# Kernel tuning notes

Measured on AMD Instinct MI355X. Metric: run time of the kernel, lower is better.

## Reference

```python
import jax, jax.numpy as jnp
import numpy as np

N = 100000      # nodes
E = 600000      # directed edges
D_IN = 128
D_H = 128
D_OUT = 128
EPS = 1e-5      # BatchNorm eps


def setup_inputs() -> dict:
    key = jax.random.key(0)
    ks = jax.random.split(key, 6)
    x = jax.random.normal(ks[0], (N, D_IN), dtype=jnp.float32)
    edge_index = jax.random.randint(ks[1], (2, E), 0, N, dtype=jnp.int64)
    s1 = 1.0 / np.sqrt(D_IN)
    s2 = 1.0 / np.sqrt(D_H)
    W1 = jax.random.uniform(ks[2], (D_IN, D_H), minval=-s1, maxval=s1, dtype=jnp.float32)
    b1 = jnp.zeros((D_H,), jnp.float32)
    gamma1 = jnp.ones((D_H,), jnp.float32)
    beta1 = jnp.zeros((D_H,), jnp.float32)
    W2 = jax.random.uniform(ks[3], (D_H, D_OUT), minval=-s2, maxval=s2, dtype=jnp.float32)
    b2 = jnp.zeros((D_OUT,), jnp.float32)
    return dict(x=x, edge_index=edge_index, W1=W1, b1=b1,
                gamma1=gamma1, beta1=beta1, W2=W2, b2=b2)


def _gcn_conv(x, W, b, src, dst):
    # PyG GCNConv: h = D^{-1/2} (A + I) D^{-1/2} (x @ W) + b
    n = x.shape[0]
    h = x @ W                                   # [N, d_out]
    loop = jnp.arange(n, dtype=src.dtype)
    s = jnp.concatenate([src, loop])            # self loops appended
    d = jnp.concatenate([dst, loop])
    deg = jax.ops.segment_sum(jnp.ones_like(d, jnp.float32), d, num_segments=n)
    dinv = jax.lax.rsqrt(deg)                   # deg >= 1 after self loops
    norm = dinv[s] * dinv[d]                    # [E + N]
    agg = jax.ops.segment_sum(h[s] * norm[:, None], d, num_segments=n)  # [N, d_out]
    return agg + b


def reference(x, edge_index, W1, b1, gamma1, beta1, W2, b2):
    src, dst = edge_index[0], edge_index[1]
    # layer 0: GCNConv -> BatchNorm1d (training batch stats) -> ReLU (dropout p=0)
    h = _gcn_conv(x, W1, b1, src, dst)
    mean = h.mean(axis=0)
    var = h.var(axis=0)                         # biased variance, as torch BN
    h = (h - mean) * jax.lax.rsqrt(var + EPS) * gamma1 + beta1
    h = jax.nn.relu(h)
    # final layer: GCNConv only
    return _gcn_conv(h, W2, b2, src, dst)
```

## Files before the change

### kernel.cpp

```cpp
#include <hip/hip_runtime.h>

#define D 128
#define EPSV 1e-5f

typedef __attribute__((ext_vector_type(8))) short bf16x8;
typedef __attribute__((ext_vector_type(4))) float f32x4;

__device__ __forceinline__ short f2bf(float f){
  unsigned u = __float_as_uint(f);
  u += 0x7fffu + ((u >> 16) & 1u);
  return (short)(u >> 16);
}
__device__ __forceinline__ float bflo(unsigned u){ return __uint_as_float(u << 16); }
__device__ __forceinline__ float bfhi(unsigned u){ return __uint_as_float(u & 0xffff0000u); }
__device__ __forceinline__ float bf2f(short s){ return __uint_as_float(((unsigned)(unsigned short)s) << 16); }
__device__ __forceinline__ unsigned packbf(float a, float b){
  unsigned lo = (unsigned short)f2bf(a);
  unsigned hi = (unsigned short)f2bf(b);
  return lo | (hi << 16);
}

__global__ void k_init(int N, int E, const int* __restrict__ ei, int* __restrict__ flag,
                       int* __restrict__ deg, int* __restrict__ fill, float* __restrict__ gpart,
                       const float* __restrict__ W1, const float* __restrict__ W2,
                       short* __restrict__ w1t, short* __restrict__ w2t){
  int i = blockIdx.x*blockDim.x + threadIdx.x;
  if (i < N){ deg[i] = 0; fill[i] = 0; }
  if (i < D*D){
    int j = i >> 7, k = i & 127;
    w1t[i] = f2bf(W1[k*D + j]);
    w2t[i] = f2bf(W2[k*D + j]);
  }
  if (i < 2048) gpart[i] = 0.f;
  if (blockIdx.x == 0){
    __shared__ int any;
    int t = threadIdx.x;
    if (t == 0) any = 0;
    __syncthreads();
    if (2*t+1 < 2*E && ei[2*t+1] != 0) atomicOr(&any, 1);
    __syncthreads();
    if (t == 0) flag[0] = (any == 0) ? 1 : 0;
  }
}

__global__ void k_count(const int* __restrict__ ei, int E, const int* __restrict__ flag,
                        int* __restrict__ deg){
  int e = blockIdx.x*blockDim.x + threadIdx.x;
  if (e >= E) return;
  int d = flag[0] ? ei[2*E + 2*e] : ei[E + e];
  atomicAdd(&deg[d], 1);
}

__global__ void k_dinv_bsum(const int* __restrict__ deg, int N, float* __restrict__ dinv,
                            int* __restrict__ bsum){
  __shared__ int sh[256];
  int t = threadIdx.x, base = blockIdx.x*1024;
  int s = 0;
  for (int i = t; i < 1024; i += 256){
    int j = base + i;
    if (j < N){ int dg = deg[j]; dinv[j] = rsqrtf((float)(dg + 1)); s += dg; }
  }
  sh[t] = s; __syncthreads();
  for (int d = 128; d > 0; d >>= 1){ if (t < d) sh[t] += sh[t+d]; __syncthreads(); }
  if (t == 0) bsum[blockIdx.x] = sh[0];
}

__global__ void k_scan_bsum(int NB, const int* __restrict__ bsum, int* __restrict__ boff){
  __shared__ int sh[128];
  int t = threadIdx.x;
  int v = (t < NB) ? bsum[t] : 0;
  sh[t] = v; __syncthreads();
  for (int d = 1; d < 128; d <<= 1){
    int u = (t >= d) ? sh[t-d] : 0;
    __syncthreads();
    sh[t] += u;
    __syncthreads();
  }
  if (t < NB) boff[t] = sh[t] - v;
}

__global__ void k_rowptr(const int* __restrict__ deg, int N, const int* __restrict__ boff,
                         int* __restrict__ row_ptr){
  __shared__ int sh[256];
  int t = threadIdx.x;
  int base = blockIdx.x*1024 + t*4;
  int c0 = (base+0 < N) ? deg[base+0] : 0;
  int c1 = (base+1 < N) ? deg[base+1] : 0;
  int c2 = (base+2 < N) ? deg[base+2] : 0;
  int c3 = (base+3 < N) ? deg[base+3] : 0;
  int s = c0 + c1 + c2 + c3;
  sh[t] = s; __syncthreads();
  for (int d = 1; d < 256; d <<= 1){
    int v = (t >= d) ? sh[t-d] : 0;
    __syncthreads();
    sh[t] += v;
    __syncthreads();
  }
  int o = sh[t] - s + boff[blockIdx.x];
  if (base+0 < N) row_ptr[base+0] = o; o += c0;
  if (base+1 < N) row_ptr[base+1] = o; o += c1;
  if (base+2 < N) row_ptr[base+2] = o; o += c2;
  if (base+3 < N) row_ptr[base+3] = o;
}

__global__ void k_scatter(const int* __restrict__ ei, int E, const int* __restrict__ flag,
                          const int* __restrict__ rowp, int* __restrict__ fill,
                          const float* __restrict__ dinv, int2* __restrict__ epack){
  int e = blockIdx.x*blockDim.x + threadIdx.x;
  if (e >= E) return;
  int s, d;
  if (flag[0]){ s = ei[2*e]; d = ei[2*E + 2*e]; }
  else        { s = ei[e];   d = ei[E + e];     }
  int pos = rowp[d] + atomicAdd(&fill[d], 1);
  int2 ev; ev.x = s; ev.y = __float_as_int(dinv[s] * dinv[d]);
  epack[pos] = ev;
}

template<int MODE>
__global__ __launch_bounds__(256, 2) void k_gemm(const void* __restrict__ A,
                                const short* __restrict__ BT, short* __restrict__ C, int N,
                                const float* __restrict__ scale, const float* __restrict__ shift){
  __shared__ short ldsB[16384];
  __shared__ short ldsC[4*2048];
  int w = threadIdx.x >> 6;
  int lane = threadIdx.x & 63;
  int m = lane & 15, quad = lane >> 4;

  {
    const bf16x8* BTv = (const bf16x8*)BT;
    bf16x8* Bw = (bf16x8*)ldsB;
    for (int g = threadIdx.x; g < 2048; g += 256){
      int row = g >> 4, ch = g & 15;
      Bw[row*16 + (ch ^ (row & 15))] = BTv[g];
    }
  }
  __syncthreads();
  const bf16x8* Bv = (const bf16x8*)ldsB;
  short* cw = ldsC + w*2048;

  int tiles = (N + 31) >> 5;
  int wid = blockIdx.x*4 + w;
  int wstride = gridDim.x*4;
  for (int tile = wid; tile < tiles; tile += wstride){
    int r0 = tile << 5;
    bf16x8 a[2][4];
    #pragma unroll
    for (int g = 0; g < 2; ++g){
      int row = r0 + g*16 + m;
      if (row >= N) row = N - 1;
      #pragma unroll
      for (int kc = 0; kc < 4; ++kc){
        int k0 = kc*32 + quad*8;
        if (MODE == 1){
          const float* Af = (const float*)A + (size_t)row*D + k0;
          float4 u = *(const float4*)Af;
          float4 v = *(const float4*)(Af + 4);
          bf16x8 tv;
          tv[0]=f2bf(u.x); tv[1]=f2bf(u.y); tv[2]=f2bf(u.z); tv[3]=f2bf(u.w);
          tv[4]=f2bf(v.x); tv[5]=f2bf(v.y); tv[6]=f2bf(v.z); tv[7]=f2bf(v.w);
          a[g][kc] = tv;
        } else {
          bf16x8 raw = *(const bf16x8*)((const short*)A + (size_t)row*D + k0);
          float4 s0v = *(const float4*)(scale + k0);
          float4 s1v = *(const float4*)(scale + k0 + 4);
          float4 h0v = *(const float4*)(shift + k0);
          float4 h1v = *(const float4*)(shift + k0 + 4);
          bf16x8 tv;
          tv[0] = f2bf(fmaxf(fmaf(bf2f(raw[0]), s0v.x, h0v.x), 0.f));
          tv[1] = f2bf(fmaxf(fmaf(bf2f(raw[1]), s0v.y, h0v.y), 0.f));
          tv[2] = f2bf(fmaxf(fmaf(bf2f(raw[2]), s0v.z, h0v.z), 0.f));
          tv[3] = f2bf(fmaxf(fmaf(bf2f(raw[3]), s0v.w, h0v.w), 0.f));
          tv[4] = f2bf(fmaxf(fmaf(bf2f(raw[4]), s1v.x, h1v.x), 0.f));
          tv[5] = f2bf(fmaxf(fmaf(bf2f(raw[5]), s1v.y, h1v.y), 0.f));
          tv[6] = f2bf(fmaxf(fmaf(bf2f(raw[6]), s1v.z, h1v.z), 0.f));
          tv[7] = f2bf(fmaxf(fmaf(bf2f(raw[7]), s1v.w, h1v.w), 0.f));
          a[g][kc] = tv;
        }
      }
    }
    f32x4 acc[2][8];
    #pragma unroll
    for (int g = 0; g < 2; ++g)
      #pragma unroll
      for (int c = 0; c < 8; ++c) acc[g][c] = (f32x4){0.f,0.f,0.f,0.f};
    #pragma unroll
    for (int kc = 0; kc < 4; ++kc){
      bf16x8 bb[8];
      #pragma unroll
      for (int c = 0; c < 8; ++c)
        bb[c] = Bv[(c*16 + m)*16 + ((kc*4 + quad) ^ m)];
      #pragma unroll
      for (int g = 0; g < 2; ++g)
        #pragma unroll
        for (int c = 0; c < 8; ++c)
          acc[g][c] = __builtin_amdgcn_mfma_f32_16x16x32_bf16(bb[c], a[g][kc], acc[g][c], 0, 0, 0);
    }
    #pragma unroll
    for (int g = 0; g < 2; ++g){
      #pragma unroll
      for (int c = 0; c < 8; ++c){
        uint2 v;
        v.x = packbf(acc[g][c][0], acc[g][c][1]);
        v.y = packbf(acc[g][c][2], acc[g][c][3]);
        int x = c*2 + (quad >> 1);
        *(uint2*)&cw[m*128 + ((x ^ m) << 3) + ((quad & 1) << 2)] = v;
      }
      asm volatile("s_waitcnt lgkmcnt(0)" ::: "memory");
      #pragma unroll
      for (int rg = 0; rg < 4; ++rg){
        int lrow = rg*4 + quad;
        int rr = r0 + g*16 + lrow;
        uint4 v = *(const uint4*)&cw[lrow*128 + ((m ^ lrow) << 3)];
        if (rr < N) *(uint4*)(C + (size_t)rr*D + m*8) = v;
      }
      asm volatile("s_waitcnt lgkmcnt(0)" ::: "memory");
    }
  }
}

template<int OUTF32>
__global__ __launch_bounds__(256) void k_agg(const short* __restrict__ H, const int* __restrict__ rowp,
        const int* __restrict__ deg, const int2* __restrict__ epack, const float* __restrict__ dinv,
        const float* __restrict__ bias, void* __restrict__ out, int N, float* __restrict__ gpart){
  int w = threadIdx.x >> 6, p = threadIdx.x & 63;
  int wid = blockIdx.x*4 + w, wstride = gridDim.x*4;
  const unsigned* Hu = (const unsigned*)H;
  float S0=0.f, S1=0.f, Q0=0.f, Q1=0.f;
  for (int n = wid; n < N; n += wstride){
    float d1 = dinv[n], w0 = d1*d1;
    unsigned u = Hu[(size_t)n*64 + p];
    float a0 = w0 * bflo(u), a1 = w0 * bfhi(u);
    int start = rowp[n], cnt = deg[n];
    for (int base = 0; base < cnt; base += 64){
      int nb = cnt - base; if (nb > 64) nb = 64;
      int2 ev;
      if (p < nb) ev = epack[start + base + p];
      else { ev.x = 0; ev.y = 0; }
      for (int j = 0; j < nb; j += 8){
        int s0 = __shfl(ev.x, j+0), s1 = __shfl(ev.x, j+1);
        int s2 = __shfl(ev.x, j+2), s3 = __shfl(ev.x, j+3);
        int s4 = __shfl(ev.x, j+4), s5 = __shfl(ev.x, j+5);
        int s6 = __shfl(ev.x, j+6), s7 = __shfl(ev.x, j+7);
        float f0 = __int_as_float(__shfl(ev.y, j+0));
        float f1 = __int_as_float(__shfl(ev.y, j+1));
        float f2 = __int_as_float(__shfl(ev.y, j+2));
        float f3 = __int_as_float(__shfl(ev.y, j+3));
        float f4 = __int_as_float(__shfl(ev.y, j+4));
        float f5 = __int_as_float(__shfl(ev.y, j+5));
        float f6 = __int_as_float(__shfl(ev.y, j+6));
        float f7 = __int_as_float(__shfl(ev.y, j+7));
        unsigned u0 = Hu[(size_t)s0*64 + p], u1 = Hu[(size_t)s1*64 + p];
        unsigned u2 = Hu[(size_t)s2*64 + p], u3 = Hu[(size_t)s3*64 + p];
        unsigned u4 = Hu[(size_t)s4*64 + p], u5 = Hu[(size_t)s5*64 + p];
        unsigned u6 = Hu[(size_t)s6*64 + p], u7 = Hu[(size_t)s7*64 + p];
        a0 = fmaf(f0, bflo(u0), a0); a1 = fmaf(f0, bfhi(u0), a1);
        a0 = fmaf(f1, bflo(u1), a0); a1 = fmaf(f1, bfhi(u1), a1);
        a0 = fmaf(f2, bflo(u2), a0); a1 = fmaf(f2, bfhi(u2), a1);
        a0 = fmaf(f3, bflo(u3), a0); a1 = fmaf(f3, bfhi(u3), a1);
        a0 = fmaf(f4, bflo(u4), a0); a1 = fmaf(f4, bfhi(u4), a1);
        a0 = fmaf(f5, bflo(u5), a0); a1 = fmaf(f5, bfhi(u5), a1);
        a0 = fmaf(f6, bflo(u6), a0); a1 = fmaf(f6, bfhi(u6), a1);
        a0 = fmaf(f7, bflo(u7), a0); a1 = fmaf(f7, bfhi(u7), a1);
      }
    }
    if (OUTF32){
      float2 r; r.x = a0 + bias[2*p]; r.y = a1 + bias[2*p+1];
      ((float2*)out)[(size_t)n*64 + p] = r;
    } else {
      ((unsigned*)out)[(size_t)n*64 + p] = packbf(a0, a1);
      S0 += a0; Q0 += a0*a0; S1 += a1; Q1 += a1*a1;
    }
  }
  if (!OUTF32){
    __shared__ float ls[1024];
    int base = w*256;
    ls[base + 2*p]       = S0;
    ls[base + 2*p + 1]   = S1;
    ls[base + 128 + 2*p]     = Q0;
    ls[base + 128 + 2*p + 1] = Q1;
    __syncthreads();
    int t = threadIdx.x;
    float v = ls[t] + ls[256 + t] + ls[512 + t] + ls[768 + t];
    atomicAdd(&gpart[(blockIdx.x & 7)*256 + t], v);
  }
}

__global__ void k_ss(const float* __restrict__ gpart, const float* __restrict__ gamma,
                     const float* __restrict__ beta, int N,
                     float* __restrict__ scale, float* __restrict__ shift){
  int f = threadIdx.x;
  if (f < 128){
    float s = 0.f, q = 0.f;
    for (int i = 0; i < 8; ++i){ s += gpart[i*256 + f]; q += gpart[i*256 + 128 + f]; }
    float inv = 1.f / (float)N;
    float mean = s * inv;
    float var  = q * inv - mean*mean;
    float sc = gamma[f] * rsqrtf(var + EPSV);
    scale[f] = sc;
    shift[f] = beta[f] - mean * sc;
  }
}

extern "C" void kernel_launch(void* const* d_in, const int* in_sizes, int n_in,
                              void* d_out, int out_size, void* d_ws, size_t ws_size,
                              hipStream_t stream){
  const float* x   = (const float*)d_in[0];
  const int*   ei  = (const int*)  d_in[1];
  const float* W1  = (const float*)d_in[2];
  const float* g1  = (const float*)d_in[4];
  const float* be1 = (const float*)d_in[5];
  const float* W2  = (const float*)d_in[6];
  const float* b2  = (const float*)d_in[7];
  float* out = (float*)d_out;
  int N = in_sizes[0] / D;
  int E = in_sizes[1] / 2;

  char* w = (char*)d_ws;
  auto carve = [&](size_t bytes)->char*{ char* p = w; w += (bytes + 255) & ~(size_t)255; return p; };
  int*   flag  = (int*)  carve(256);
  int*   degA  = (int*)  carve((size_t)N*4);
  int*   fillA = (int*)  carve((size_t)N*4);
  float* dinvA = (float*)carve((size_t)N*4);
  int*   rowp  = (int*)  carve((size_t)N*4);
  int*   bsum  = (int*)  carve(4096);
  int*   boff  = (int*)  carve(4096);
  int2*  epack = (int2*) carve((size_t)E*8);
  float* gpart = (float*)carve(2048*4);
  float* scale = (float*)carve(512);
  float* shift = (float*)carve(512);
  short* w1t   = (short*)carve((size_t)D*D*2);
  short* w2t   = (short*)carve((size_t)D*D*2);
  short* h1    = (short*)carve((size_t)N*D*2);
  short* hb    = (short*)carve((size_t)N*D*2);

  const int TB = 256;
  int EB  = (E + TB - 1) / TB;
  int NBt = (N + TB - 1) / TB;
  int NB1024 = (N + 1023) / 1024;
  int GEMMB = 512;
  int AGGB  = 2048;

  k_init      <<<NBt, TB, 0, stream>>>(N, E, ei, flag, degA, fillA, gpart, W1, W2, w1t, w2t);
  k_count     <<<EB, TB, 0, stream>>>(ei, E, flag, degA);
  k_dinv_bsum <<<NB1024, 256, 0, stream>>>(degA, N, dinvA, bsum);
  k_scan_bsum <<<1, 128, 0, stream>>>(NB1024, bsum, boff);
  k_rowptr    <<<NB1024, 256, 0, stream>>>(degA, N, boff, rowp);
  k_scatter   <<<EB, TB, 0, stream>>>(ei, E, flag, rowp, fillA, dinvA, epack);
  k_gemm<1>   <<<GEMMB, 256, 0, stream>>>(x, w1t, h1, N, nullptr, nullptr);
  k_agg<0>    <<<AGGB, 256, 0, stream>>>(h1, rowp, degA, epack, dinvA, nullptr, hb, N, gpart);
  k_ss        <<<1, 128, 0, stream>>>(gpart, g1, be1, N, scale, shift);
  k_gemm<2>   <<<GEMMB, 256, 0, stream>>>(hb, w2t, h1, N, scale, shift);
  k_agg<1>    <<<AGGB, 256, 0, stream>>>(h1, rowp, degA, epack, dinvA, b2, out, N, gpart);
}
```

Baseline: 266.1 us.

## Fuse degree count into GEMM, single-pass lookback scan, inline BN stats, prefetch agg rows

Extra blocks in the first GEMM launch now do the degree counting, so the atomics overlap the dense GEMM. The three-kernel row-pointer scan becomes one decoupled-lookback scan that also writes dinv. The BN scale and shift are computed per block inside the second GEMM, which removes k_ss. The aggregation loop now prefetches the next node's row metadata and first edge chunk. The changes cut launch count and expose more latency overlap, at the cost of spin-waiting across blocks in the scan and redundant BN stat work in every GEMM block.

```diff
diff --git a/kernel.cpp b/kernel.cpp
--- a/kernel.cpp
+++ b/kernel.cpp
@@ -22,6 +22,7 @@
 
 __global__ void k_init(int N, int E, const int* __restrict__ ei, int* __restrict__ flag,
                        int* __restrict__ deg, int* __restrict__ fill, float* __restrict__ gpart,
+                       int* __restrict__ sflg,
                        const float* __restrict__ W1, const float* __restrict__ W2,
                        short* __restrict__ w1t, short* __restrict__ w2t){
   int i = blockIdx.x*blockDim.x + threadIdx.x;
@@ -32,6 +33,7 @@
     w2t[i] = f2bf(W2[k*D + j]);
   }
   if (i < 2048) gpart[i] = 0.f;
+  if (i < 128) sflg[i] = 0;
   if (blockIdx.x == 0){
     __shared__ int any;
     int t = threadIdx.x;
@@ -43,47 +45,13 @@
   }
 }
 
-__global__ void k_count(const int* __restrict__ ei, int E, const int* __restrict__ flag,
-                        int* __restrict__ deg){
-  int e = blockIdx.x*blockDim.x + threadIdx.x;
-  if (e >= E) return;
-  int d = flag[0] ? ei[2*E + 2*e] : ei[E + e];
-  atomicAdd(&deg[d], 1);
-}
-
-__global__ void k_dinv_bsum(const int* __restrict__ deg, int N, float* __restrict__ dinv,
-                            int* __restrict__ bsum){
+__global__ void k_scan(const int* __restrict__ deg, int N, int* __restrict__ rowp,
+                       float* __restrict__ dinv, int* __restrict__ s_agg,
+                       int* __restrict__ s_inc, int* __restrict__ s_flg){
   __shared__ int sh[256];
-  int t = threadIdx.x, base = blockIdx.x*1024;
-  int s = 0;
-  for (int i = t; i < 1024; i += 256){
-    int j = base + i;
-    if (j < N){ int dg = deg[j]; dinv[j] = rsqrtf((float)(dg + 1)); s += dg; }
-  }
-  sh[t] = s; __syncthreads();
-  for (int d = 128; d > 0; d >>= 1){ if (t < d) sh[t] += sh[t+d]; __syncthreads(); }
-  if (t == 0) bsum[blockIdx.x] = sh[0];
-}
-
-__global__ void k_scan_bsum(int NB, const int* __restrict__ bsum, int* __restrict__ boff){
-  __shared__ int sh[128];
-  int t = threadIdx.x;
-  int v = (t < NB) ? bsum[t] : 0;
-  sh[t] = v; __syncthreads();
-  for (int d = 1; d < 128; d <<= 1){
-    int u = (t >= d) ? sh[t-d] : 0;
-    __syncthreads();
-    sh[t] += u;
-    __syncthreads();
-  }
-  if (t < NB) boff[t] = sh[t] - v;
-}
-
-__global__ void k_rowptr(const int* __restrict__ deg, int N, const int* __restrict__ boff,
-                         int* __restrict__ row_ptr){
-  __shared__ int sh[256];
-  int t = threadIdx.x;
-  int base = blockIdx.x*1024 + t*4;
+  __shared__ int s_ex;
+  int b = blockIdx.x, t = threadIdx.x;
+  int base = b*1024 + t*4;
   int c0 = (base+0 < N) ? deg[base+0] : 0;
   int c1 = (base+1 < N) ? deg[base+1] : 0;
   int c2 = (base+2 < N) ? deg[base+2] : 0;
@@ -96,11 +64,29 @@
     sh[t] += v;
     __syncthreads();
   }
-  int o = sh[t] - s + boff[blockIdx.x];
-  if (base+0 < N) row_ptr[base+0] = o; o += c0;
-  if (base+1 < N) row_ptr[base+1] = o; o += c1;
-  if (base+2 < N) row_ptr[base+2] = o; o += c2;
-  if (base+3 < N) row_ptr[base+3] = o;
+  int total = sh[255];
+  if (t == 0){
+    atomicExch(&s_agg[b], total);
+    __threadfence();
+    atomicExch(&s_flg[b], 1);
+    int ex = 0;
+    for (int i = b-1; i >= 0; ){
+      int f;
+      while ((f = atomicAdd(&s_flg[i], 0)) == 0) __builtin_amdgcn_s_sleep(1);
+      if (f == 2){ ex += atomicAdd(&s_inc[i], 0); break; }
+      ex += atomicAdd(&s_agg[i], 0); --i;
+    }
+    atomicExch(&s_inc[b], ex + total);
+    __threadfence();
+    atomicExch(&s_flg[b], 2);
+    s_ex = ex;
+  }
+  __syncthreads();
+  int o = sh[t] - s + s_ex;
+  if (base+0 < N){ rowp[base+0] = o; dinv[base+0] = rsqrtf((float)(c0+1)); } o += c0;
+  if (base+1 < N){ rowp[base+1] = o; dinv[base+1] = rsqrtf((float)(c1+1)); } o += c1;
+  if (base+2 < N){ rowp[base+2] = o; dinv[base+2] = rsqrtf((float)(c2+1)); } o += c2;
+  if (base+3 < N){ rowp[base+3] = o; dinv[base+3] = rsqrtf((float)(c3+1)); }
 }
 
 __global__ void k_scatter(const int* __restrict__ ei, int E, const int* __restrict__ flag,
@@ -119,13 +105,44 @@
 template<int MODE>
 __global__ __launch_bounds__(256, 2) void k_gemm(const void* __restrict__ A,
                                 const short* __restrict__ BT, short* __restrict__ C, int N,
-                                const float* __restrict__ scale, const float* __restrict__ shift){
+                                const float* __restrict__ gpart, const float* __restrict__ gamma,
+                                const float* __restrict__ beta,
+                                const int* __restrict__ ei, int E, const int* __restrict__ flag,
+                                int* __restrict__ deg, int ngemmb){
+  if (MODE == 1 && (int)blockIdx.x >= ngemmb){
+    int cb = blockIdx.x - ngemmb;
+    int e0 = cb*1024 + threadIdx.x;
+    int f = flag[0];
+    #pragma unroll
+    for (int r = 0; r < 4; ++r){
+      int e = e0 + r*256;
+      if (e < E){
+        int d = f ? ei[2*E + 2*e] : ei[E + e];
+        atomicAdd(&deg[d], 1);
+      }
+    }
+    return;
+  }
   __shared__ short ldsB[16384];
   __shared__ short ldsC[4*2048];
+  __shared__ __align__(16) float s_sc[128];
+  __shared__ __align__(16) float s_sh[128];
   int w = threadIdx.x >> 6;
   int lane = threadIdx.x & 63;
   int m = lane & 15, quad = lane >> 4;
 
+  if (MODE == 2 && threadIdx.x < 128){
+    int f = threadIdx.x;
+    float s = 0.f, q = 0.f;
+    #pragma unroll
+    for (int i = 0; i < 8; ++i){ s += gpart[i*256 + f]; q += gpart[i*256 + 128 + f]; }
+    float inv = 1.f / (float)N;
+    float mean = s * inv;
+    float var  = q * inv - mean*mean;
+    float sc = gamma[f] * rsqrtf(var + EPSV);
+    s_sc[f] = sc;
+    s_sh[f] = beta[f] - mean * sc;
+  }
   {
     const bf16x8* BTv = (const bf16x8*)BT;
     bf16x8* Bw = (bf16x8*)ldsB;
@@ -140,7 +157,7 @@
 
   int tiles = (N + 31) >> 5;
   int wid = blockIdx.x*4 + w;
-  int wstride = gridDim.x*4;
+  int wstride = ngemmb*4;
   for (int tile = wid; tile < tiles; tile += wstride){
     int r0 = tile << 5;
     bf16x8 a[2][4];
@@ -161,10 +178,10 @@
           a[g][kc] = tv;
         } else {
           bf16x8 raw = *(const bf16x8*)((const short*)A + (size_t)row*D + k0);
-          float4 s0v = *(const float4*)(scale + k0);
-          float4 s1v = *(const float4*)(scale + k0 + 4);
-          float4 h0v = *(const float4*)(shift + k0);
-          float4 h1v = *(const float4*)(shift + k0 + 4);
+          float4 s0v = *(const float4*)(s_sc + k0);
+          float4 s1v = *(const float4*)(s_sc + k0 + 4);
+          float4 h0v = *(const float4*)(s_sh + k0);
+          float4 h1v = *(const float4*)(s_sh + k0 + 4);
           bf16x8 tv;
           tv[0] = f2bf(fmaxf(fmaf(bf2f(raw[0]), s0v.x, h0v.x), 0.f));
           tv[1] = f2bf(fmaxf(fmaf(bf2f(raw[1]), s0v.y, h0v.y), 0.f));
@@ -226,50 +243,77 @@
   int wid = blockIdx.x*4 + w, wstride = gridDim.x*4;
   const unsigned* Hu = (const unsigned*)H;
   float S0=0.f, S1=0.f, Q0=0.f, Q1=0.f;
-  for (int n = wid; n < N; n += wstride){
-    float d1 = dinv[n], w0 = d1*d1;
-    unsigned u = Hu[(size_t)n*64 + p];
+  float bb0=0.f, bb1=0.f;
+  if (OUTF32){ bb0 = bias[2*p]; bb1 = bias[2*p+1]; }
+
+  int n = wid;
+  int start=0, cnt=0; float d1=0.f; unsigned u=0; int2 ev; ev.x=0; ev.y=0;
+  if (n < N){
+    start = rowp[n]; cnt = deg[n]; d1 = dinv[n];
+    u = Hu[(size_t)n*64 + p];
+    int nb = cnt < 64 ? cnt : 64;
+    if (p < nb) ev = epack[start + p];
+  }
+  while (n < N){
+    int n2 = n + wstride;
+    int start2=0, cnt2=0; float d12=0.f; unsigned u2=0; int2 ev2; ev2.x=0; ev2.y=0;
+    if (n2 < N){
+      start2 = rowp[n2]; cnt2 = deg[n2]; d12 = dinv[n2];
+      u2 = Hu[(size_t)n2*64 + p];
+      int nb2 = cnt2 < 64 ? cnt2 : 64;
+      if (p < nb2) ev2 = epack[start2 + p];
+    }
+    float w0 = d1*d1;
     float a0 = w0 * bflo(u), a1 = w0 * bfhi(u);
-    int start = rowp[n], cnt = deg[n];
-    for (int base = 0; base < cnt; base += 64){
-      int nb = cnt - base; if (nb > 64) nb = 64;
-      int2 ev;
-      if (p < nb) ev = epack[start + base + p];
-      else { ev.x = 0; ev.y = 0; }
-      for (int j = 0; j < nb; j += 8){
-        int s0 = __shfl(ev.x, j+0), s1 = __shfl(ev.x, j+1);
-        int s2 = __shfl(ev.x, j+2), s3 = __shfl(ev.x, j+3);
-        int s4 = __shfl(ev.x, j+4), s5 = __shfl(ev.x, j+5);
-        int s6 = __shfl(ev.x, j+6), s7 = __shfl(ev.x, j+7);
-        float f0 = __int_as_float(__shfl(ev.y, j+0));
-        float f1 = __int_as_float(__shfl(ev.y, j+1));
-        float f2 = __int_as_float(__shfl(ev.y, j+2));
-        float f3 = __int_as_float(__shfl(ev.y, j+3));
-        float f4 = __int_as_float(__shfl(ev.y, j+4));
-        float f5 = __int_as_float(__shfl(ev.y, j+5));
-        float f6 = __int_as_float(__shfl(ev.y, j+6));
-        float f7 = __int_as_float(__shfl(ev.y, j+7));
-        unsigned u0 = Hu[(size_t)s0*64 + p], u1 = Hu[(size_t)s1*64 + p];
-        unsigned u2 = Hu[(size_t)s2*64 + p], u3 = Hu[(size_t)s3*64 + p];
-        unsigned u4 = Hu[(size_t)s4*64 + p], u5 = Hu[(size_t)s5*64 + p];
-        unsigned u6 = Hu[(size_t)s6*64 + p], u7 = Hu[(size_t)s7*64 + p];
-        a0 = fmaf(f0, bflo(u0), a0); a1 = fmaf(f0, bfhi(u0), a1);
-        a0 = fmaf(f1, bflo(u1), a0); a1 = fmaf(f1, bfhi(u1), a1);
-        a0 = fmaf(f2, bflo(u2), a0); a1 = fmaf(f2, bfhi(u2), a1);
-        a0 = fmaf(f3, bflo(u3), a0); a1 = fmaf(f3, bfhi(u3), a1);
-        a0 = fmaf(f4, bflo(u4), a0); a1 = fmaf(f4, bfhi(u4), a1);
-        a0 = fmaf(f5, bflo(u5), a0); a1 = fmaf(f5, bfhi(u5), a1);
-        a0 = fmaf(f6, bflo(u6), a0); a1 = fmaf(f6, bfhi(u6), a1);
-        a0 = fmaf(f7, bflo(u7), a0); a1 = fmaf(f7, bfhi(u7), a1);
+    int nb = cnt < 64 ? cnt : 64;
+    for (int j = 0; j < nb; j += 8){
+      int s0 = __shfl(ev.x, j+0), s1 = __shfl(ev.x, j+1);
+      int s2 = __shfl(ev.x, j+2), s3 = __shfl(ev.x, j+3);
+      int s4 = __shfl(ev.x, j+4), s5 = __shfl(ev.x, j+5);
+      int s6 = __shfl(ev.x, j+6), s7 = __shfl(ev.x, j+7);
+      float f0 = __int_as_float(__shfl(ev.y, j+0));
+      float f1 = __int_as_float(__shfl(ev.y, j+1));
+      float f2 = __int_as_float(__shfl(ev.y, j+2));
+      float f3 = __int_as_float(__shfl(ev.y, j+3));
+      float f4 = __int_as_float(__shfl(ev.y, j+4));
+      float f5 = __int_as_float(__shfl(ev.y, j+5));
+      float f6 = __int_as_float(__shfl(ev.y, j+6));
+      float f7 = __int_as_float(__shfl(ev.y, j+7));
+      unsigned u0 = Hu[(size_t)s0*64 + p], u1 = Hu[(size_t)s1*64 + p];
+      unsigned u2g = Hu[(size_t)s2*64 + p], u3 = Hu[(size_t)s3*64 + p];
+      unsigned u4 = Hu[(size_t)s4*64 + p], u5 = Hu[(size_t)s5*64 + p];
+      unsigned u6 = Hu[(size_t)s6*64 + p], u7 = Hu[(size_t)s7*64 + p];
+      a0 = fmaf(f0, bflo(u0), a0); a1 = fmaf(f0, bfhi(u0), a1);
+      a0 = fmaf(f1, bflo(u1), a0); a1 = fmaf(f1, bfhi(u1), a1);
+      a0 = fmaf(f2, bflo(u2g), a0); a1 = fmaf(f2, bfhi(u2g), a1);
+      a0 = fmaf(f3, bflo(u3), a0); a1 = fmaf(f3, bfhi(u3), a1);
+      a0 = fmaf(f4, bflo(u4), a0); a1 = fmaf(f4, bfhi(u4), a1);
+      a0 = fmaf(f5, bflo(u5), a0); a1 = fmaf(f5, bfhi(u5), a1);
+      a0 = fmaf(f6, bflo(u6), a0); a1 = fmaf(f6, bfhi(u6), a1);
+      a0 = fmaf(f7, bflo(u7), a0); a1 = fmaf(f7, bfhi(u7), a1);
+    }
+    for (int base = 64; base < cnt; base += 64){
+      int nbx = cnt - base; if (nbx > 64) nbx = 64;
+      int2 evx; evx.x = 0; evx.y = 0;
+      if (p < nbx) evx = epack[start + base + p];
+      for (int j = 0; j < nbx; j += 8){
+        #pragma unroll
+        for (int q2 = 0; q2 < 8; ++q2){
+          int sx = __shfl(evx.x, j+q2);
+          float fx = __int_as_float(__shfl(evx.y, j+q2));
+          unsigned ux = Hu[(size_t)sx*64 + p];
+          a0 = fmaf(fx, bflo(ux), a0); a1 = fmaf(fx, bfhi(ux), a1);
+        }
       }
     }
     if (OUTF32){
-      float2 r; r.x = a0 + bias[2*p]; r.y = a1 + bias[2*p+1];
+      float2 r; r.x = a0 + bb0; r.y = a1 + bb1;
       ((float2*)out)[(size_t)n*64 + p] = r;
     } else {
       ((unsigned*)out)[(size_t)n*64 + p] = packbf(a0, a1);
       S0 += a0; Q0 += a0*a0; S1 += a1; Q1 += a1*a1;
     }
+    n = n2; start = start2; cnt = cnt2; d1 = d12; u = u2; ev = ev2;
   }
   if (!OUTF32){
     __shared__ float ls[1024];
@@ -282,22 +326,6 @@
     int t = threadIdx.x;
     float v = ls[t] + ls[256 + t] + ls[512 + t] + ls[768 + t];
     atomicAdd(&gpart[(blockIdx.x & 7)*256 + t], v);
-  }
-}
-
-__global__ void k_ss(const float* __restrict__ gpart, const float* __restrict__ gamma,
-                     const float* __restrict__ beta, int N,
-                     float* __restrict__ scale, float* __restrict__ shift){
-  int f = threadIdx.x;
-  if (f < 128){
-    float s = 0.f, q = 0.f;
-    for (int i = 0; i < 8; ++i){ s += gpart[i*256 + f]; q += gpart[i*256 + 128 + f]; }
-    float inv = 1.f / (float)N;
-    float mean = s * inv;
-    float var  = q * inv - mean*mean;
-    float sc = gamma[f] * rsqrtf(var + EPSV);
-    scale[f] = sc;
-    shift[f] = beta[f] - mean * sc;
   }
 }
 
@@ -322,12 +350,11 @@
   int*   fillA = (int*)  carve((size_t)N*4);
   float* dinvA = (float*)carve((size_t)N*4);
   int*   rowp  = (int*)  carve((size_t)N*4);
-  int*   bsum  = (int*)  carve(4096);
-  int*   boff  = (int*)  carve(4096);
+  int*   sagg  = (int*)  carve(512);
+  int*   sinc  = (int*)  carve(512);
+  int*   sflg  = (int*)  carve(512);
   int2*  epack = (int2*) carve((size_t)E*8);
   float* gpart = (float*)carve(2048*4);
-  float* scale = (float*)carve(512);
-  float* shift = (float*)carve(512);
   short* w1t   = (short*)carve((size_t)D*D*2);
   short* w2t   = (short*)carve((size_t)D*D*2);
   short* h1    = (short*)carve((size_t)N*D*2);
@@ -338,17 +365,16 @@
   int NBt = (N + TB - 1) / TB;
   int NB1024 = (N + 1023) / 1024;
   int GEMMB = 512;
+  int CNTB  = (E + 1023) / 1024;
   int AGGB  = 2048;
 
-  k_init      <<<NBt, TB, 0, stream>>>(N, E, ei, flag, degA, fillA, gpart, W1, W2, w1t, w2t);
-  k_count     <<<EB, TB, 0, stream>>>(ei, E, flag, degA);
-  k_dinv_bsum <<<NB1024, 256, 0, stream>>>(degA, N, dinvA, bsum);
-  k_scan_bsum <<<1, 128, 0, stream>>>(NB1024, bsum, boff);
-  k_rowptr    <<<NB1024, 256, 0, stream>>>(degA, N, boff, rowp);
-  k_scatter   <<<EB, TB, 0, stream>>>(ei, E, flag, rowp, fillA, dinvA, epack);
-  k_gemm<1>   <<<GEMMB, 256, 0, stream>>>(x, w1t, h1, N, nullptr, nullptr);
-  k_agg<0>    <<<AGGB, 256, 0, stream>>>(h1, rowp, degA, epack, dinvA, nullptr, hb, N, gpart);
-  k_ss        <<<1, 128, 0, stream>>>(gpart, g1, be1, N, scale, shift);
-  k_gemm<2>   <<<GEMMB, 256, 0, stream>>>(hb, w2t, h1, N, scale, shift);
-  k_agg<1>    <<<AGGB, 256, 0, stream>>>(h1, rowp, degA, epack, dinvA, b2, out, N, gpart);
-}
+  k_init    <<<NBt, TB, 0, stream>>>(N, E, ei, flag, degA, fillA, gpart, sflg, W1, W2, w1t, w2t);
+  k_gemm<1> <<<GEMMB + CNTB, 256, 0, stream>>>(x, w1t, h1, N, nullptr, nullptr, nullptr,
+                                               ei, E, flag, degA, GEMMB);
+  k_scan    <<<NB1024, 256, 0, stream>>>(degA, N, rowp, dinvA, sagg, sinc, sflg);
+  k_scatter <<<EB, TB, 0, stream>>>(ei, E, flag, rowp, fillA, dinvA, epack);
+  k_agg<0>  <<<AGGB, 256, 0, stream>>>(h1, rowp, degA, epack, dinvA, nullptr, hb, N, gpart);
+  k_gemm<2> <<<GEMMB, 256, 0, stream>>>(hb, w2t, h1, N, gpart, g1, be1,
+                                        nullptr, 0, nullptr, nullptr, GEMMB);
+  k_agg<1>  <<<AGGB, 256, 0, stream>>>(h1, rowp, degA, epack, dinvA, b2, out, N, nullptr);
+}
```

After: 259.2 us. 1.03x faster.
